# Kernel tuning notes

Measured on AMD Instinct MI355X. Metric: run time of the kernel, lower is better.

Reference implementation:

```python
import jax, jax.numpy as jnp
import numpy as np

N_POS = 1024
ALPHA = 0.3
B, S = 32, 1024


def setup_inputs() -> dict:
    key = jax.random.key(0)
    k1, k2, k3, k4 = jax.random.split(key, 4)
    s_arc = jax.random.normal(k1, (B, S, S), dtype=jnp.float32)
    a_arc = jax.random.normal(k2, (B, S, S), dtype=jnp.float32)
    adds = jax.random.randint(k3, (B, S), 0, N_POS, dtype=jnp.int32)
    pos = jax.random.randint(k4, (B, S), 0, N_POS, dtype=jnp.int32)
    return {"s_arc": s_arc, "a_arc": a_arc, "adds": adds, "pos": pos}


def reference(s_arc, a_arc, adds, pos):
    n_bins = N_POS * N_POS
    # --- histogram (scatter-add) of a_arc by POS-pair index ---
    # original: _add[b,p1,p2] = adds[b,p1]*seq_len + adds[b,p2]
    sl = adds.shape[1]
    pair_idx = adds[:, :, None] * sl + adds[:, None, :]            # [B,S,S]
    # indices >= n_bins never match any bin in the original masked-sum loop;
    # segment_sum with num_segments=n_bins drops them identically.
    hist = jax.ops.segment_sum(a_arc.reshape(-1), pair_idx.reshape(-1),
                               num_segments=n_bins)                # [n_pos^2]
    score_arc = jax.nn.sigmoid(hist)
    # --- gather score back into s_arc ---
    slp = pos.shape[1]
    pidx = pos[:, :, None] * slp + pos[:, None, :]                  # [B,S,S]
    valid = pidx < n_bins
    gathered = score_arc[jnp.clip(pidx, 0, n_bins - 1)]
    return s_arc + ALPHA * jnp.where(valid, gathered, jnp.float32(0))
```

## Files before the change

### kernel.cpp

```cpp
#include <hip/hip_runtime.h>

#define NPOS 1024
#define BB   32
#define SS   1024
#define ALPHA_C 0.3f
#define OCAP 1024
#define MAXO 16
#define PADPAIR 0x10001000u
#define SSTRIDE 1026

__global__ __launch_bounds__(256) void zero_fill(float4* __restrict__ p) {
    p[blockIdx.x * 256 + threadIdx.x] = make_float4(0.f, 0.f, 0.f, 0.f);
}

__global__ __launch_bounds__(1024) void build_tables(
    const int* __restrict__ adds, unsigned* __restrict__ rcnt,
    unsigned* __restrict__ bmask, ushort* __restrict__ list,
    ushort* __restrict__ ell16, int* __restrict__ ocntc, int* __restrict__ ocntr,
    int* __restrict__ oentc, int* __restrict__ oentr) {
    __shared__ int scnt[NPOS];
    __shared__ int soc, sor;
    const int b = blockIdx.x, t = threadIdx.x;
    const int c = adds[b * SS + t];
    ((uint2*)ell16)[b * 1024 + t] = make_uint2(PADPAIR, PADPAIR);
    scnt[t] = 0;
    if (t == 0) { soc = 0; sor = 0; }
    __syncthreads();
    const int slot = atomicAdd(&scnt[c], 1);
    if (slot < 4) {
        ell16[(((size_t)b * 512 + (c & 511)) * 2 + (c >> 9)) * 4 + slot] = (ushort)(t << 2);
    } else {
        const int o = atomicAdd(&soc, 1);
        if (o < OCAP) oentc[b * OCAP + o] = (c << 10) | t;
    }
    const unsigned rs = atomicAdd(&rcnt[c * BB + b], 1u);
    if (rs < 4) {
        list[(size_t)c * 128 + b * 4 + rs] = (ushort)t;
    } else {
        const int o = atomicAdd(&sor, 1);
        if (o < OCAP) oentr[b * OCAP + o] = (c << 10) | t;
        atomicOr(&bmask[b * 32 + (t >> 5)], 1u << (t & 31));
    }
    __syncthreads();
    if (t == 0) { ocntc[b] = min(soc, OCAP); ocntr[b] = min(sor, OCAP); }
}

__global__ __launch_bounds__(256) void fixup(
    const float* __restrict__ a, const int* __restrict__ adds,
    const int* __restrict__ ocntc, const int* __restrict__ oentc,
    const int* __restrict__ ocntr, const int* __restrict__ oentr,
    const unsigned* __restrict__ bmask, float* __restrict__ hist) {
    const int b = blockIdx.x;
    int y = blockIdx.y;
    const int p = blockIdx.z * 256 + threadIdx.x;
    if (y < MAXO) {
        if (y >= ocntc[b]) return;
        const int e = oentc[b * OCAP + y];
        const int c = e >> 10, p2 = e & 1023;
        if ((bmask[b * 32 + (p >> 5)] >> (p & 31)) & 1u) return;
        const int r = adds[b * SS + p];
        atomicAdd(&hist[(size_t)r * NPOS + c], a[((size_t)(b * SS + p)) * SS + p2]);
    } else {
        y -= MAXO;
        if (y >= ocntr[b]) return;
        const int e = oentr[b * OCAP + y];
        const int r = e >> 10, p1 = e & 1023;
        const int c = adds[b * SS + p];
        atomicAdd(&hist[(size_t)r * NPOS + c], a[((size_t)(b * SS + p1)) * SS + p]);
    }
}

__global__ __launch_bounds__(512) void hist_rows_kernel(
    const float* __restrict__ a, const unsigned* __restrict__ rcnt,
    const ushort* __restrict__ list, const ushort* __restrict__ ell16,
    float* __restrict__ hist) {
    __shared__ float Sbuf[2][SSTRIDE];
    __shared__ ushort lsrc[128];
    __shared__ int   mcnt_s[32];
    __shared__ ushort actb_s[32];
    __shared__ int   na_s;
    const int r = blockIdx.x, t = threadIdx.x;

    if (t < 128) lsrc[t] = list[(size_t)r * 128 + t];
    if (t < 32)  mcnt_s[t] = min((int)rcnt[r * BB + t], 4);
    if (t < 2)   Sbuf[t][1024] = 0.f;
    __syncthreads();
    if (t == 0) {
        int na = 0;
        for (int b = 0; b < 32; ++b) if (mcnt_s[b]) actb_s[na++] = (ushort)b;
        na_s = na;
    }
    __syncthreads();
    const int na = na_s;
    const uint4* ellv = (const uint4*)ell16;
    float acc0 = 0.f, acc1 = 0.f;
    uint4 E = make_uint4(PADPAIR, PADPAIR, PADPAIR, PADPAIR), F = E;
    float2 R0 = make_float2(0.f, 0.f), R1 = R0, R2 = R0, R3 = R0;
    int mNext = 0;

#define ROWP(bb, s) ((const float2*)(a + ((((size_t)(bb) << 10) + lsrc[(bb) * 4 + (s)]) << 10)) + t)

    if (na > 0) {
        const int b0 = actb_s[0], m0 = mcnt_s[b0];
        E = ellv[(size_t)b0 * 512 + t];
        float2 S = *ROWP(b0, 0);
        if (m0 > 1) { float2 x = *ROWP(b0, 1); S.x += x.x; S.y += x.y; }
        if (m0 > 2) { float2 x = *ROWP(b0, 2); S.x += x.x; S.y += x.y; }
        if (m0 > 3) { float2 x = *ROWP(b0, 3); S.x += x.x; S.y += x.y; }
        ((float2*)&Sbuf[0][0])[t] = S;
        if (na > 1) {
            const int b1 = actb_s[1];
            mNext = mcnt_s[b1];
            F = ellv[(size_t)b1 * 512 + t];
            R0 = *ROWP(b1, 0);
            if (mNext > 1) R1 = *ROWP(b1, 1);
            if (mNext > 2) R2 = *ROWP(b1, 2);
            if (mNext > 3) R3 = *ROWP(b1, 3);
        }
    }
    asm volatile("s_waitcnt lgkmcnt(0)" ::: "memory");
    __builtin_amdgcn_s_barrier();

    for (int j = 0; j < na; ++j) {
        float2 T0 = make_float2(0.f, 0.f), T1 = T0, T2 = T0, T3 = T0;
        uint4 TE = make_uint4(PADPAIR, PADPAIR, PADPAIR, PADPAIR);
        int mIn = 0;
        if (j + 2 < na) {
            const int b2 = actb_s[j + 2];
            mIn = mcnt_s[b2];
            TE = ellv[(size_t)b2 * 512 + t];
            T0 = *ROWP(b2, 0);
            if (mIn > 1) T1 = *ROWP(b2, 1);
            if (mIn > 2) T2 = *ROWP(b2, 2);
            if (mIn > 3) T3 = *ROWP(b2, 3);
        }
        if (j + 1 < na) {
            float2 S = R0;
            if (mNext > 1) { S.x += R1.x; S.y += R1.y; }
            if (mNext > 2) { S.x += R2.x; S.y += R2.y; }
            if (mNext > 3) { S.x += R3.x; S.y += R3.y; }
            ((float2*)&Sbuf[(j + 1) & 1][0])[t] = S;
        }
        const char* rb = (const char*)&Sbuf[j & 1][0];
        acc0 += *(const float*)(rb + (E.x & 0xffffu));
        acc0 += *(const float*)(rb + (E.x >> 16));
        acc0 += *(const float*)(rb + (E.y & 0xffffu));
        acc0 += *(const float*)(rb + (E.y >> 16));
        acc1 += *(const float*)(rb + (E.z & 0xffffu));
        acc1 += *(const float*)(rb + (E.z >> 16));
        acc1 += *(const float*)(rb + (E.w & 0xffffu));
        acc1 += *(const float*)(rb + (E.w >> 16));
        E = F; F = TE;
        R0 = T0; R1 = T1; R2 = T2; R3 = T3; mNext = mIn;
        __builtin_amdgcn_sched_barrier(0);
        asm volatile("s_waitcnt lgkmcnt(0)" ::: "memory");
        __builtin_amdgcn_s_barrier();
    }
#undef ROWP

    const size_t o0 = (size_t)r * NPOS + t;
    const float base0 = hist[o0], base1 = hist[o0 + 512];
    hist[o0]       = 1.f / (1.f + __expf(-(base0 + acc0)));
    hist[o0 + 512] = 1.f / (1.f + __expf(-(base1 + acc1)));
}

__global__ __launch_bounds__(256) void gather_kernel(
    const float* __restrict__ s, const int* __restrict__ pos,
    const float* __restrict__ score, float* __restrict__ out) {
    const int row = blockIdx.x;
    const int b   = row >> 10;
    const int*  posb = pos + b * SS;
    const int   base = posb[row & 1023] * NPOS;
    const size_t off = (size_t)row * SS;

    const int t = threadIdx.x;
    float4 v = ((const float4*)(s + off))[t];
    int4   c = ((const int4*)posb)[t];
    float4 o;
    o.x = v.x + ALPHA_C * score[base + c.x];
    o.y = v.y + ALPHA_C * score[base + c.y];
    o.z = v.z + ALPHA_C * score[base + c.z];
    o.w = v.w + ALPHA_C * score[base + c.w];
    ((float4*)(out + off))[t] = o;
}

extern "C" void kernel_launch(void* const* d_in, const int* in_sizes, int n_in,
                              void* d_out, int out_size, void* d_ws, size_t ws_size,
                              hipStream_t stream) {
    const float* s_arc = (const float*)d_in[0];
    const float* a_arc = (const float*)d_in[1];
    const int*   adds  = (const int*)d_in[2];
    const int*   pos   = (const int*)d_in[3];
    float* out  = (float*)d_out;

    char* w = (char*)d_ws;
    float*    hist  = (float*)w;                 w += (size_t)NPOS * NPOS * 4;
    unsigned* rcnt  = (unsigned*)w;              w += (size_t)NPOS * BB * 4;
    unsigned* bmask = (unsigned*)w;              w += (size_t)BB * 32 * 4;
    ushort*   list  = (ushort*)w;                w += (size_t)NPOS * 128 * 2;
    ushort*   ell16 = (ushort*)w;                w += (size_t)BB * NPOS * 4 * 2;
    int*      ocntc = (int*)w;                   w += BB * 4;
    int*      ocntr = (int*)w;                   w += BB * 4;
    int*      oentc = (int*)w;                   w += (size_t)BB * OCAP * 4;
    int*      oentr = (int*)w;

    zero_fill<<<1057, 256, 0, stream>>>((float4*)hist);
    build_tables<<<BB, 1024, 0, stream>>>(adds, rcnt, bmask, list, ell16,
                                          ocntc, ocntr, oentc, oentr);
    fixup<<<dim3(BB, 2 * MAXO, SS / 256), 256, 0, stream>>>(a_arc, adds, ocntc, oentc,
                                                            ocntr, oentr, bmask, hist);
    hist_rows_kernel<<<NPOS, 512, 0, stream>>>(a_arc, rcnt, list, ell16, hist);
    gather_kernel<<<BB * SS, 256, 0, stream>>>(s_arc, pos, hist, out);
}
```

Measured before the change: 132.7 us.

## Drop hist zero-fill, move sigmoid into gather, split table build across blocks

The 4 MB zero-fill of the histogram is removed. hist_rows_kernel now writes raw sums directly, and fixup runs afterwards to atomically add the overflow entries. Sigmoid is applied per element in gather_kernel instead of once per bin, and table building is spread over 4x more blocks using global per-batch counters that a combined fill kernel zeroes. Nontemporal loads and stores are added for the streamed arrays, and OCAP is reduced. The cost is 32M expf evaluations in gather instead of 1M, and a tighter overflow capacity.

```diff
diff --git a/kernel.cpp b/kernel.cpp
--- a/kernel.cpp
+++ b/kernel.cpp
@@ -4,45 +4,142 @@
 #define BB   32
 #define SS   1024
 #define ALPHA_C 0.3f
-#define OCAP 1024
+#define OCAP 256
 #define MAXO 16
 #define PADPAIR 0x10001000u
 #define SSTRIDE 1026
-
-__global__ __launch_bounds__(256) void zero_fill(float4* __restrict__ p) {
-    p[blockIdx.x * 256 + threadIdx.x] = make_float4(0.f, 0.f, 0.f, 0.f);
-}
-
-__global__ __launch_bounds__(1024) void build_tables(
+#define NZ4 16656
+#define NP4 16384
+
+typedef float    __attribute__((ext_vector_type(2))) f32x2;
+typedef float    __attribute__((ext_vector_type(4))) f32x4;
+typedef int      __attribute__((ext_vector_type(4))) i32x4;
+typedef unsigned __attribute__((ext_vector_type(4))) u32x4;
+
+__global__ __launch_bounds__(256) void fill_tables(u32x4* __restrict__ z,
+                                                   u32x4* __restrict__ p) {
+    const int i = blockIdx.x * 256 + threadIdx.x;
+    if (i < NZ4) z[i] = (u32x4){0u, 0u, 0u, 0u};
+    else { const int j = i - NZ4; if (j < NP4) p[j] = (u32x4){PADPAIR, PADPAIR, PADPAIR, PADPAIR}; }
+}
+
+__global__ __launch_bounds__(256) void build_tables(
     const int* __restrict__ adds, unsigned* __restrict__ rcnt,
-    unsigned* __restrict__ bmask, ushort* __restrict__ list,
-    ushort* __restrict__ ell16, int* __restrict__ ocntc, int* __restrict__ ocntr,
+    unsigned* __restrict__ scnt, unsigned* __restrict__ bmask,
+    ushort* __restrict__ list, ushort* __restrict__ ell16,
+    int* __restrict__ ocntc, int* __restrict__ ocntr,
     int* __restrict__ oentc, int* __restrict__ oentr) {
-    __shared__ int scnt[NPOS];
-    __shared__ int soc, sor;
-    const int b = blockIdx.x, t = threadIdx.x;
-    const int c = adds[b * SS + t];
-    ((uint2*)ell16)[b * 1024 + t] = make_uint2(PADPAIR, PADPAIR);
-    scnt[t] = 0;
-    if (t == 0) { soc = 0; sor = 0; }
+    const int b  = blockIdx.x >> 2;
+    const int tg = ((blockIdx.x & 3) << 8) | threadIdx.x;
+    const int c  = adds[b * SS + tg];
+    const unsigned slot = atomicAdd(&scnt[b * NPOS + c], 1u);
+    if (slot < 4u) {
+        ell16[(((size_t)b * 512 + (c & 511)) * 2 + (c >> 9)) * 4 + slot] = (ushort)(tg << 2);
+    } else {
+        const int o = atomicAdd(&ocntc[b], 1);
+        if (o < OCAP) oentc[b * OCAP + o] = (c << 10) | tg;
+    }
+    const unsigned rs = atomicAdd(&rcnt[c * BB + b], 1u);
+    if (rs < 4u) {
+        list[(size_t)c * 128 + b * 4 + rs] = (ushort)tg;
+    } else {
+        const int o = atomicAdd(&ocntr[b], 1);
+        if (o < OCAP) oentr[b * OCAP + o] = (c << 10) | tg;
+        atomicOr(&bmask[b * 32 + (tg >> 5)], 1u << (tg & 31));
+    }
+}
+
+__global__ __launch_bounds__(512) void hist_rows_kernel(
+    const float* __restrict__ a, const unsigned* __restrict__ rcnt,
+    const ushort* __restrict__ list, const ushort* __restrict__ ell16,
+    float* __restrict__ hist) {
+    __shared__ float Sbuf[2][SSTRIDE];
+    __shared__ ushort lsrc[128];
+    __shared__ int   mcnt_s[32];
+    __shared__ ushort actb_s[32];
+    __shared__ int   na_s;
+    const int r = blockIdx.x, t = threadIdx.x;
+
+    if (t < 128) lsrc[t] = list[(size_t)r * 128 + t];
+    if (t < 32)  mcnt_s[t] = min((int)rcnt[r * BB + t], 4);
+    if (t < 2)   Sbuf[t][1024] = 0.f;
     __syncthreads();
-    const int slot = atomicAdd(&scnt[c], 1);
-    if (slot < 4) {
-        ell16[(((size_t)b * 512 + (c & 511)) * 2 + (c >> 9)) * 4 + slot] = (ushort)(t << 2);
-    } else {
-        const int o = atomicAdd(&soc, 1);
-        if (o < OCAP) oentc[b * OCAP + o] = (c << 10) | t;
-    }
-    const unsigned rs = atomicAdd(&rcnt[c * BB + b], 1u);
-    if (rs < 4) {
-        list[(size_t)c * 128 + b * 4 + rs] = (ushort)t;
-    } else {
-        const int o = atomicAdd(&sor, 1);
-        if (o < OCAP) oentr[b * OCAP + o] = (c << 10) | t;
-        atomicOr(&bmask[b * 32 + (t >> 5)], 1u << (t & 31));
+    if (t == 0) {
+        int na = 0;
+        for (int b = 0; b < 32; ++b) if (mcnt_s[b]) actb_s[na++] = (ushort)b;
+        na_s = na;
     }
     __syncthreads();
-    if (t == 0) { ocntc[b] = min(soc, OCAP); ocntr[b] = min(sor, OCAP); }
+    const int na = na_s;
+    const u32x4* ellv = (const u32x4*)ell16;
+    float acc0 = 0.f, acc1 = 0.f;
+    u32x4 E = (u32x4){PADPAIR, PADPAIR, PADPAIR, PADPAIR}, F = E;
+    f32x2 R0 = (f32x2){0.f, 0.f}, R1 = R0, R2 = R0, R3 = R0;
+    int mNext = 0;
+
+#define ROWP(bb, s) ((const f32x2*)(a + ((((size_t)(bb) << 10) + lsrc[(bb) * 4 + (s)]) << 10)) + t)
+
+    if (na > 0) {
+        const int b0 = actb_s[0], m0 = mcnt_s[b0];
+        E = ellv[(size_t)b0 * 512 + t];
+        f32x2 S = __builtin_nontemporal_load(ROWP(b0, 0));
+        if (m0 > 1) S += __builtin_nontemporal_load(ROWP(b0, 1));
+        if (m0 > 2) S += __builtin_nontemporal_load(ROWP(b0, 2));
+        if (m0 > 3) S += __builtin_nontemporal_load(ROWP(b0, 3));
+        ((f32x2*)&Sbuf[0][0])[t] = S;
+        if (na > 1) {
+            const int b1 = actb_s[1];
+            mNext = mcnt_s[b1];
+            F = ellv[(size_t)b1 * 512 + t];
+            R0 = __builtin_nontemporal_load(ROWP(b1, 0));
+            if (mNext > 1) R1 = __builtin_nontemporal_load(ROWP(b1, 1));
+            if (mNext > 2) R2 = __builtin_nontemporal_load(ROWP(b1, 2));
+            if (mNext > 3) R3 = __builtin_nontemporal_load(ROWP(b1, 3));
+        }
+    }
+    asm volatile("s_waitcnt lgkmcnt(0)" ::: "memory");
+    __builtin_amdgcn_s_barrier();
+
+    for (int j = 0; j < na; ++j) {
+        f32x2 T0 = (f32x2){0.f, 0.f}, T1 = T0, T2 = T0, T3 = T0;
+        u32x4 TE = (u32x4){PADPAIR, PADPAIR, PADPAIR, PADPAIR};
+        int mIn = 0;
+        if (j + 2 < na) {
+            const int b2 = actb_s[j + 2];
+            mIn = mcnt_s[b2];
+            TE = ellv[(size_t)b2 * 512 + t];
+            T0 = __builtin_nontemporal_load(ROWP(b2, 0));
+            if (mIn > 1) T1 = __builtin_nontemporal_load(ROWP(b2, 1));
+            if (mIn > 2) T2 = __builtin_nontemporal_load(ROWP(b2, 2));
+            if (mIn > 3) T3 = __builtin_nontemporal_load(ROWP(b2, 3));
+        }
+        if (j + 1 < na) {
+            f32x2 S = R0;
+            if (mNext > 1) S += R1;
+            if (mNext > 2) S += R2;
+            if (mNext > 3) S += R3;
+            ((f32x2*)&Sbuf[(j + 1) & 1][0])[t] = S;
+        }
+        const char* rb = (const char*)&Sbuf[j & 1][0];
+        acc0 += *(const float*)(rb + (E.x & 0xffffu));
+        acc0 += *(const float*)(rb + (E.x >> 16));
+        acc0 += *(const float*)(rb + (E.y & 0xffffu));
+        acc0 += *(const float*)(rb + (E.y >> 16));
+        acc1 += *(const float*)(rb + (E.z & 0xffffu));
+        acc1 += *(const float*)(rb + (E.z >> 16));
+        acc1 += *(const float*)(rb + (E.w & 0xffffu));
+        acc1 += *(const float*)(rb + (E.w >> 16));
+        E = F; F = TE;
+        R0 = T0; R1 = T1; R2 = T2; R3 = T3; mNext = mIn;
+        __builtin_amdgcn_sched_barrier(0);
+        asm volatile("s_waitcnt lgkmcnt(0)" ::: "memory");
+        __builtin_amdgcn_s_barrier();
+    }
+#undef ROWP
+
+    const size_t o0 = (size_t)r * NPOS + t;
+    hist[o0]       = acc0;
+    hist[o0 + 512] = acc1;
 }
 
 __global__ __launch_bounds__(256) void fixup(
@@ -70,100 +167,6 @@
     }
 }
 
-__global__ __launch_bounds__(512) void hist_rows_kernel(
-    const float* __restrict__ a, const unsigned* __restrict__ rcnt,
-    const ushort* __restrict__ list, const ushort* __restrict__ ell16,
-    float* __restrict__ hist) {
-    __shared__ float Sbuf[2][SSTRIDE];
-    __shared__ ushort lsrc[128];
-    __shared__ int   mcnt_s[32];
-    __shared__ ushort actb_s[32];
-    __shared__ int   na_s;
-    const int r = blockIdx.x, t = threadIdx.x;
-
-    if (t < 128) lsrc[t] = list[(size_t)r * 128 + t];
-    if (t < 32)  mcnt_s[t] = min((int)rcnt[r * BB + t], 4);
-    if (t < 2)   Sbuf[t][1024] = 0.f;
-    __syncthreads();
-    if (t == 0) {
-        int na = 0;
-        for (int b = 0; b < 32; ++b) if (mcnt_s[b]) actb_s[na++] = (ushort)b;
-        na_s = na;
-    }
-    __syncthreads();
-    const int na = na_s;
-    const uint4* ellv = (const uint4*)ell16;
-    float acc0 = 0.f, acc1 = 0.f;
-    uint4 E = make_uint4(PADPAIR, PADPAIR, PADPAIR, PADPAIR), F = E;
-    float2 R0 = make_float2(0.f, 0.f), R1 = R0, R2 = R0, R3 = R0;
-    int mNext = 0;
-
-#define ROWP(bb, s) ((const float2*)(a + ((((size_t)(bb) << 10) + lsrc[(bb) * 4 + (s)]) << 10)) + t)
-
-    if (na > 0) {
-        const int b0 = actb_s[0], m0 = mcnt_s[b0];
-        E = ellv[(size_t)b0 * 512 + t];
-        float2 S = *ROWP(b0, 0);
-        if (m0 > 1) { float2 x = *ROWP(b0, 1); S.x += x.x; S.y += x.y; }
-        if (m0 > 2) { float2 x = *ROWP(b0, 2); S.x += x.x; S.y += x.y; }
-        if (m0 > 3) { float2 x = *ROWP(b0, 3); S.x += x.x; S.y += x.y; }
-        ((float2*)&Sbuf[0][0])[t] = S;
-        if (na > 1) {
-            const int b1 = actb_s[1];
-            mNext = mcnt_s[b1];
-            F = ellv[(size_t)b1 * 512 + t];
-            R0 = *ROWP(b1, 0);
-            if (mNext > 1) R1 = *ROWP(b1, 1);
-            if (mNext > 2) R2 = *ROWP(b1, 2);
-            if (mNext > 3) R3 = *ROWP(b1, 3);
-        }
-    }
-    asm volatile("s_waitcnt lgkmcnt(0)" ::: "memory");
-    __builtin_amdgcn_s_barrier();
-
-    for (int j = 0; j < na; ++j) {
-        float2 T0 = make_float2(0.f, 0.f), T1 = T0, T2 = T0, T3 = T0;
-        uint4 TE = make_uint4(PADPAIR, PADPAIR, PADPAIR, PADPAIR);
-        int mIn = 0;
-        if (j + 2 < na) {
-            const int b2 = actb_s[j + 2];
-            mIn = mcnt_s[b2];
-            TE = ellv[(size_t)b2 * 512 + t];
-            T0 = *ROWP(b2, 0);
-            if (mIn > 1) T1 = *ROWP(b2, 1);
-            if (mIn > 2) T2 = *ROWP(b2, 2);
-            if (mIn > 3) T3 = *ROWP(b2, 3);
-        }
-        if (j + 1 < na) {
-            float2 S = R0;
-            if (mNext > 1) { S.x += R1.x; S.y += R1.y; }
-            if (mNext > 2) { S.x += R2.x; S.y += R2.y; }
-            if (mNext > 3) { S.x += R3.x; S.y += R3.y; }
-            ((float2*)&Sbuf[(j + 1) & 1][0])[t] = S;
-        }
-        const char* rb = (const char*)&Sbuf[j & 1][0];
-        acc0 += *(const float*)(rb + (E.x & 0xffffu));
-        acc0 += *(const float*)(rb + (E.x >> 16));
-        acc0 += *(const float*)(rb + (E.y & 0xffffu));
-        acc0 += *(const float*)(rb + (E.y >> 16));
-        acc1 += *(const float*)(rb + (E.z & 0xffffu));
-        acc1 += *(const float*)(rb + (E.z >> 16));
-        acc1 += *(const float*)(rb + (E.w & 0xffffu));
-        acc1 += *(const float*)(rb + (E.w >> 16));
-        E = F; F = TE;
-        R0 = T0; R1 = T1; R2 = T2; R3 = T3; mNext = mIn;
-        __builtin_amdgcn_sched_barrier(0);
-        asm volatile("s_waitcnt lgkmcnt(0)" ::: "memory");
-        __builtin_amdgcn_s_barrier();
-    }
-#undef ROWP
-
-    const size_t o0 = (size_t)r * NPOS + t;
-    const float base0 = hist[o0], base1 = hist[o0 + 512];
-    hist[o0]       = 1.f / (1.f + __expf(-(base0 + acc0)));
-    hist[o0 + 512] = 1.f / (1.f + __expf(-(base1 + acc1)));
-}
-
 __global__ __launch_bounds__(256) void gather_kernel(
     const float* __restrict__ s, const int* __restrict__ pos,
     const float* __restrict__ score, float* __restrict__ out) {
@@ -174,14 +177,16 @@
     const size_t off = (size_t)row * SS;
 
     const int t = threadIdx.x;
-    float4 v = ((const float4*)(s + off))[t];
-    int4   c = ((const int4*)posb)[t];
-    float4 o;
-    o.x = v.x + ALPHA_C * score[base + c.x];
-    o.y = v.y + ALPHA_C * score[base + c.y];
-    o.z = v.z + ALPHA_C * score[base + c.z];
-    o.w = v.w + ALPHA_C * score[base + c.w];
-    ((float4*)(out + off))[t] = o;
+    f32x4 v = __builtin_nontemporal_load(((const f32x4*)(s + off)) + t);
+    i32x4 c = ((const i32x4*)posb)[t];
+    const float h0 = score[base + c.x], h1 = score[base + c.y];
+    const float h2 = score[base + c.z], h3 = score[base + c.w];
+    f32x4 o;
+    o.x = v.x + ALPHA_C * (1.f / (1.f + __expf(-h0)));
+    o.y = v.y + ALPHA_C * (1.f / (1.f + __expf(-h1)));
+    o.z = v.z + ALPHA_C * (1.f / (1.f + __expf(-h2)));
+    o.w = v.w + ALPHA_C * (1.f / (1.f + __expf(-h3)));
+    __builtin_nontemporal_store(o, ((f32x4*)(out + off)) + t);
 }
 
 extern "C" void kernel_launch(void* const* d_in, const int* in_sizes, int n_in,
@@ -196,19 +201,20 @@
     char* w = (char*)d_ws;
     float*    hist  = (float*)w;                 w += (size_t)NPOS * NPOS * 4;
     unsigned* rcnt  = (unsigned*)w;              w += (size_t)NPOS * BB * 4;
+    unsigned* scnt  = (unsigned*)w;              w += (size_t)BB * NPOS * 4;
     unsigned* bmask = (unsigned*)w;              w += (size_t)BB * 32 * 4;
+    int*      ocntc = (int*)w;                   w += BB * 4;
+    int*      ocntr = (int*)w;                   w += BB * 4;
     ushort*   list  = (ushort*)w;                w += (size_t)NPOS * 128 * 2;
     ushort*   ell16 = (ushort*)w;                w += (size_t)BB * NPOS * 4 * 2;
-    int*      ocntc = (int*)w;                   w += BB * 4;
-    int*      ocntr = (int*)w;                   w += BB * 4;
     int*      oentc = (int*)w;                   w += (size_t)BB * OCAP * 4;
     int*      oentr = (int*)w;
 
-    zero_fill<<<1057, 256, 0, stream>>>((float4*)hist);
-    build_tables<<<BB, 1024, 0, stream>>>(adds, rcnt, bmask, list, ell16,
-                                          ocntc, ocntr, oentc, oentr);
+    fill_tables<<<(NZ4 + NP4 + 255) / 256, 256, 0, stream>>>((u32x4*)rcnt, (u32x4*)ell16);
+    build_tables<<<4 * BB, 256, 0, stream>>>(adds, rcnt, scnt, bmask, list, ell16,
+                                             ocntc, ocntr, oentc, oentr);
+    hist_rows_kernel<<<NPOS, 512, 0, stream>>>(a_arc, rcnt, list, ell16, hist);
     fixup<<<dim3(BB, 2 * MAXO, SS / 256), 256, 0, stream>>>(a_arc, adds, ocntc, oentc,
                                                             ocntr, oentr, bmask, hist);
-    hist_rows_kernel<<<NPOS, 512, 0, stream>>>(a_arc, rcnt, list, ell16, hist);
     gather_kernel<<<BB * SS, 256, 0, stream>>>(s_arc, pos, hist, out);
 }
```

Result: no change. 131.7 us (-0.8%).
